# Kernel optimization log

Measured on AMD Instinct MI355X. Metric: run time of the kernel, lower is better.

Reference implementation:

```python
import jax, jax.numpy as jnp
import numpy as np

B, S, E, H = 4, 4096, 1024, 16
D = E // H  # head_dim = 64


def _xavier(key, out_f, in_f):
    lim = float(np.sqrt(6.0 / (in_f + out_f)))
    return jax.random.uniform(key, (out_f, in_f), jnp.float32, -lim, lim)


def setup_inputs() -> dict:
    key = jax.random.key(0)
    ks = jax.random.split(key, 9)
    x = jax.random.normal(ks[0], (B, S, E), jnp.float32)
    Wq = _xavier(ks[1], E, E)
    Wk = _xavier(ks[2], E, E)
    Wv = _xavier(ks[3], E, E)
    Wo = _xavier(ks[4], E, E)
    bq = jnp.zeros((E,), jnp.float32)
    bk = jnp.zeros((E,), jnp.float32)
    bv = jnp.zeros((E,), jnp.float32)
    bo = jnp.zeros((E,), jnp.float32)
    return {"x": x, "Wq": Wq, "bq": bq, "Wk": Wk, "bk": bk,
            "Wv": Wv, "bv": bv, "Wo": Wo, "bo": bo}


def _feature_map(t):
    # elu(t) + 1 (positive feature map)
    return jax.nn.elu(t) + 1.0


def reference(x, Wq, bq, Wk, bk, Wv, bv, Wo, bo):
    b, s, _ = x.shape
    # projections (torch Linear: y = x @ W.T + b), reshape to [b, s, h, d]
    Q = (x @ Wq.T + bq).reshape(b, s, H, D)
    K = (x @ Wk.T + bk).reshape(b, s, H, D)
    V = (x @ Wv.T + bv).reshape(b, s, H, D)
    Q = _feature_map(Q)
    K = _feature_map(K)
    # KV summary: [b, h, d, e]
    KV = jnp.einsum('bshd,bshe->bhde', K, V)
    K_sum = K.sum(axis=1)  # [b, h, d]
    Z = 1.0 / (jnp.einsum('bshd,bhd->bsh', Q, K_sum) + 1e-6)  # [b, s, h]
    out = jnp.einsum('bshd,bhde,bsh->bshe', Q, KV, Z)  # [b, s, h, e]
    out = out.reshape(b, s, E)
    out = out @ Wo.T + bo
    return out
```

## Files before the change

kernel.cpp:

```cpp
#include <hip/hip_runtime.h>
#include <math.h>

#define BB 4
#define SS 4096
#define EE 1024
#define HH 16
#define DD 64
#define MM (BB*SS)

typedef _Float16 f16x8 __attribute__((ext_vector_type(8)));
typedef _Float16 f16x4 __attribute__((ext_vector_type(4)));
typedef float    f32x4 __attribute__((ext_vector_type(4)));

typedef __attribute__((address_space(3))) void lds_void;
typedef __attribute__((address_space(1))) void gm_void;

__device__ __forceinline__ void gload16(const void* g, void* l) {
  __builtin_amdgcn_global_load_lds((gm_void*)g, (lds_void*)l, 16, 0, 0);
}

__global__ __launch_bounds__(256) void conv_x_kernel(const float* __restrict__ x,
                                                     _Float16* __restrict__ xh, int n4) {
  int i = blockIdx.x * blockDim.x + threadIdx.x;
  int stride = gridDim.x * blockDim.x;
  for (; i < n4; i += stride) {
    f32x4 v = *(const f32x4*)&x[(size_t)i * 4];
    f16x4 h;
    h[0] = (_Float16)v[0]; h[1] = (_Float16)v[1];
    h[2] = (_Float16)v[2]; h[3] = (_Float16)v[3];
    *(f16x4*)&xh[(size_t)i * 4] = h;
  }
}

__global__ __launch_bounds__(256) void conv_w_kernel(const float* __restrict__ Wq,
                                                     const float* __restrict__ Wk,
                                                     const float* __restrict__ Wv,
                                                     const float* __restrict__ Wo,
                                                     _Float16* __restrict__ wqkv,
                                                     _Float16* __restrict__ woh) {
  const int per = (EE * EE) / 4;
  int i = blockIdx.x * blockDim.x + threadIdx.x;
  int stride = gridDim.x * blockDim.x;
  for (; i < 4 * per; i += stride) {
    int seg = i / per, off = i - seg * per;
    const float* src = (seg == 0) ? Wq : (seg == 1) ? Wk : (seg == 2) ? Wv : Wo;
    _Float16* dst = (seg < 3) ? (wqkv + (size_t)seg * EE * EE) : woh;
    f32x4 v = *(const f32x4*)&src[(size_t)off * 4];
    f16x4 h;
    h[0] = (_Float16)v[0]; h[1] = (_Float16)v[1];
    h[2] = (_Float16)v[2]; h[3] = (_Float16)v[3];
    *(f16x4*)&dst[(size_t)off * 4] = h;
  }
}


#define SB0() __builtin_amdgcn_sched_barrier(0)
#define VMW6 asm volatile("s_waitcnt vmcnt(6)" ::: "memory")
#define VMW0 asm volatile("s_waitcnt vmcnt(0)" ::: "memory")
#define NOP_ do {} while (0)

#define STAGE_M(Gb, Lb, t, hf) do {                                          \
    const char* g_ = (Gb) + ((size_t)(hf) << 18) + (size_t)(t) * 128;        \
    char* d_ = (Lb) + (((t) & 1) << 15) + ((hf) << 14) + dsub;               \
    gload16(g_, d_);                                                         \
    gload16(g_ + ((size_t)64 << 11), d_ + 8192);                             \
  } while (0)

#define STAGE_A(t, hf) STAGE_M(Ag, Asb, t, hf)
#define STAGE_B(t, hf) STAGE_M(Bg, Bsb, t, hf)

#define RD_A(mf, s) (*(const f16x8*)(Asb + buf_ +                            \
    (((((mf) < 4) ? 0 : 8) + wr4 + ((mf) & 3)) << 11) + ((s) << 10) + lof))
#define RD_B(nf, s) (*(const f16x8*)(Bsb + buf_ + ((wc4 + (nf)) << 11) + ((s) << 10) + lof))

#define PHASE(t, P, STG, VMC) do {                                           \
    const int buf_ = ((t) & 1) << 15;                                        \
    if ((P) == 0) {                                                          \
      _Pragma("unroll") for (int nf = 0; nf < 4; nf++) {                     \
        b[nf][0] = RD_B(nf, 0); b[nf][1] = RD_B(nf, 1);                      \
      }                                                                      \
    }                                                                        \
    aP[0][0] = RD_A((P) * 2, 0);     aP[0][1] = RD_A((P) * 2, 1);            \
    aP[1][0] = RD_A((P) * 2 + 1, 0); aP[1][1] = RD_A((P) * 2 + 1, 1);        \
    STG;                                                                     \
    SB0(); __builtin_amdgcn_s_barrier(); SB0();                              \
    asm volatile("s_waitcnt lgkmcnt(0)" ::: "memory"); SB0();                \
    __builtin_amdgcn_s_setprio(1);                                           \
    _Pragma("unroll") for (int nf = 0; nf < 4; nf++) {                       \
      acc[(P)*2][nf]   = __builtin_amdgcn_mfma_f32_16x16x32_f16(aP[0][0], b[nf][0], acc[(P)*2][nf], 0, 0, 0);   \
      acc[(P)*2][nf]   = __builtin_amdgcn_mfma_f32_16x16x32_f16(aP[0][1], b[nf][1], acc[(P)*2][nf], 0, 0, 0);   \
      acc[(P)*2+1][nf] = __builtin_amdgcn_mfma_f32_16x16x32_f16(aP[1][0], b[nf][0], acc[(P)*2+1][nf], 0, 0, 0); \
      acc[(P)*2+1][nf] = __builtin_amdgcn_mfma_f32_16x16x32_f16(aP[1][1], b[nf][1], acc[(P)*2+1][nf], 0, 0, 0); \
    }                                                                        \
    __builtin_amdgcn_s_setprio(0);                                           \
    VMC;                                                                     \
    SB0(); __builtin_amdgcn_s_barrier(); SB0();                              \
  } while (0)

#define TILE(t, S1, S2, S3, S4, VMC) do {                                    \
    PHASE(t, 0, S1, NOP_);                                                   \
    PHASE(t, 1, S2, NOP_);                                                   \
    PHASE(t, 2, S3, NOP_);                                                   \
    PHASE(t, 3, S4, VMC);                                                    \
  } while (0)

template <int EPI>
__global__ __launch_bounds__(512, 2) void gemm256(const _Float16* __restrict__ A,
                                                  const _Float16* __restrict__ Bw,
                                                  const float* __restrict__ bias0,
                                                  const float* __restrict__ bias1,
                                                  const float* __restrict__ bias2,
                                                  _Float16* __restrict__ O0,
                                                  _Float16* __restrict__ O1,
                                                  _Float16* __restrict__ O2,
                                                  float* __restrict__ OF) {
  __shared__ __align__(16) char lds[131072];
  char* Asb = lds;
  char* Bsb = lds + 65536;

  const int tid  = threadIdx.x;
  const int lane = tid & 63;
  const int wv   = tid >> 6;
  const int wr4  = (wv >> 2) << 2;
  const int wc4  = (wv & 3) << 2;
  const int wrow = (wv >> 2) << 6;
  const int wcol = (wv & 3) << 6;

  constexpr int NX = (EPI == 0) ? 12 : 4;
  const int q = (int)gridDim.x >> 3;
  const int bid = (int)blockIdx.x;
  const int sid = (bid & 7) * q + (bid >> 3);
  const int mbase = (sid / NX) << 8;
  const int nbase = (sid % NX) << 8;

  const int lof   = (((lane & 15) << 6) | ((lane >> 4) << 4)) ^ ((lane & 8) << 2);
  const int srow  = lane >> 2;
  const int sbyte = ((lane & 3) << 4) ^ (lane & 32);

  const int rg   = wv >> 1;
  const int kgs  = wv & 1;
  const int dsub = ((rg << 1) + kgs) << 10;

  const char* Ag = (const char*)A +
      ((size_t)(mbase + (rg << 4) + srow) << 11) + (kgs << 6) + sbyte;
  const char* Bg = (const char*)Bw +
      ((size_t)(nbase + (rg << 4) + srow) << 11) + (kgs << 6) + sbyte;

  f32x4 acc[8][4] = {};
  f16x8 b[4][2];
  f16x8 aP[2][2];

  STAGE_A(0, 0); STAGE_A(0, 1);
  STAGE_B(0, 0); STAGE_B(0, 1);
  STAGE_B(1, 0); STAGE_B(1, 1);
  STAGE_A(1, 0);
  VMW6;
  SB0(); __builtin_amdgcn_s_barrier(); SB0();

#pragma unroll 1
  for (int i = 0; i < 7; ++i) {
    const int t = i << 1;
    TILE(t,     STAGE_A(t + 1, 1), STAGE_B(t + 2, 0), STAGE_B(t + 2, 1), STAGE_A(t + 2, 0), VMW6);
    TILE(t + 1, STAGE_A(t + 2, 1), STAGE_B(t + 3, 0), STAGE_B(t + 3, 1), STAGE_A(t + 3, 0), VMW6);
  }
  TILE(14, STAGE_A(15, 1), NOP_, NOP_, NOP_, VMW0);
  TILE(15, NOP_, NOP_, NOP_, NOP_, NOP_);

  const int rl = (lane >> 4) << 2;
  const int cl = lane & 15;
  if (EPI == 0) {
    const int which = nbase >> 10;
    const float* bias = (which == 0) ? bias0 : (which == 1) ? bias1 : bias2;
    _Float16* O = (which == 0) ? O0 : (which == 1) ? O1 : O2;
    const int cb = (nbase & 1023) + wcol;
#pragma unroll
    for (int mf = 0; mf < 8; mf++) {
      const int gm = mbase + ((mf < 4) ? 0 : 128) + wrow + ((mf & 3) << 4) + rl;
#pragma unroll
      for (int nf = 0; nf < 4; nf++) {
        const int gc = cb + (nf << 4) + cl;
        const float bz = bias[gc];
#pragma unroll
        for (int j = 0; j < 4; j++) {
          float v = acc[mf][nf][j] + bz;
          if (which < 2) v = (v > 0.f) ? (v + 1.f) : expf(v);
          O[(size_t)(gm + j) * EE + gc] = (_Float16)v;
        }
      }
    }
  } else {
    const int cb = nbase + wcol;
#pragma unroll
    for (int mf = 0; mf < 8; mf++) {
      const int gm = mbase + ((mf < 4) ? 0 : 128) + wrow + ((mf & 3) << 4) + rl;
#pragma unroll
      for (int nf = 0; nf < 4; nf++) {
        const int gc = cb + (nf << 4) + cl;
        const float bz = bias0[gc];
#pragma unroll
        for (int j = 0; j < 4; j++)
          OF[(size_t)(gm + j) * EE + gc] = acc[mf][nf][j] + bz;
      }
    }
  }
}

#undef TILE
#undef PHASE
#undef RD_A
#undef RD_B
#undef STAGE_A
#undef STAGE_B
#undef STAGE_M

__global__ __launch_bounds__(256) void kv_partial_kernel(const _Float16* __restrict__ Kh,
                                                         const _Float16* __restrict__ Vh,
                                                         float* __restrict__ kvpart,
                                                         float* __restrict__ ksump) {
  __shared__ __align__(16) _Float16 Ks[64 * 64];
  __shared__ __align__(16) _Float16 Vs[64 * 64];
  const int tid = threadIdx.x;
  const int wv = tid >> 6;
  const int bh = blockIdx.x;
  const int chunk = blockIdx.y;
  const int b = bh >> 4, h = bh & 15;
  const int td = tid >> 4, te = tid & 15;
  const int d0 = td * 4, e0 = te * 4;

  float kv[4][4] = {};
  float ks4[4] = {0.f, 0.f, 0.f, 0.f};

  for (int sub = 0; sub < 4; sub++) {
    const int s0 = chunk * 256 + sub * 64;
    __syncthreads();
    {
      const int g0 = tid, g1 = tid + 256;
      gload16((const char*)Kh + ((size_t)(b * SS + s0 + (g0 >> 3)) * EE + h * DD) * 2 + (g0 & 7) * 16,
              (char*)Ks + wv * 1024);
      gload16((const char*)Kh + ((size_t)(b * SS + s0 + (g1 >> 3)) * EE + h * DD) * 2 + (g1 & 7) * 16,
              (char*)Ks + 4096 + wv * 1024);
      gload16((const char*)Vh + ((size_t)(b * SS + s0 + (g0 >> 3)) * EE + h * DD) * 2 + (g0 & 7) * 16,
              (char*)Vs + wv * 1024);
      gload16((const char*)Vh + ((size_t)(b * SS + s0 + (g1 >> 3)) * EE + h * DD) * 2 + (g1 & 7) * 16,
              (char*)Vs + 4096 + wv * 1024);
    }
    __syncthreads();
#pragma unroll 8
    for (int s = 0; s < 64; s++) {
      f16x4 kk = *(const f16x4*)&Ks[s * 64 + d0];
      f16x4 vv = *(const f16x4*)&Vs[s * 64 + e0];
      float kf[4], vf[4];
#pragma unroll
      for (int i = 0; i < 4; i++) { kf[i] = (float)kk[i]; vf[i] = (float)vv[i]; }
#pragma unroll
      for (int i = 0; i < 4; i++)
#pragma unroll
        for (int j = 0; j < 4; j++) kv[i][j] += kf[i] * vf[j];
      if (te == 0) {
#pragma unroll
        for (int i = 0; i < 4; i++) ks4[i] += kf[i];
      }
    }
  }
  const size_t base = ((size_t)chunk * 64 + bh) * 4096;
#pragma unroll
  for (int i = 0; i < 4; i++)
#pragma unroll
    for (int j = 0; j < 4; j++) kvpart[base + (size_t)(d0 + i) * 64 + e0 + j] = kv[i][j];
  if (te == 0) {
#pragma unroll
    for (int i = 0; i < 4; i++) ksump[((size_t)chunk * 64 + bh) * 64 + d0 + i] = ks4[i];
  }
}

__global__ __launch_bounds__(256) void kv_reduce_kernel(const float* __restrict__ kvpart,
                                                        const float* __restrict__ ksump,
                                                        _Float16* __restrict__ kvt,
                                                        float* __restrict__ ksum) {
  const int idx = blockIdx.x * 256 + threadIdx.x;
  if (blockIdx.x < 1024) {
    const int bh = idx >> 12;
    const int rem = idx & 4095;
    float s = 0.f;
#pragma unroll
    for (int c = 0; c < 16; c++) s += kvpart[((size_t)c * 64 + bh) * 4096 + rem];
    const int d = rem >> 6, e = rem & 63;
    kvt[(size_t)bh * 4096 + e * 64 + d] = (_Float16)s;
  } else {
    const int i2 = idx - 1024 * 256;
    const int bh = i2 >> 6, d = i2 & 63;
    float s = 0.f;
#pragma unroll
    for (int c = 0; c < 16; c++) s += ksump[((size_t)c * 64 + bh) * 64 + d];
    ksum[i2] = s;
  }
}

__global__ __launch_bounds__(256) void attn_kernel(const _Float16* __restrict__ Qh,
                                                   const _Float16* __restrict__ kvt,
                                                   const float* __restrict__ ksum,
                                                   _Float16* __restrict__ attn) {
  __shared__ __align__(16) _Float16 Qs[64 * 64];
  __shared__ __align__(16) _Float16 KVs[64 * 64];
  __shared__ float ks_lds[64];
  __shared__ float dpart[4][64];
  __shared__ float zr[64];
  const int tid = threadIdx.x;
  const int lane = tid & 63;
  const int wv = tid >> 6;
  const int stile = blockIdx.x;
  const int bh = blockIdx.y;
  const int b = bh >> 4, h = bh & 15;
  const int m0 = b * SS + stile * 64;

  {
    const int g0 = tid, g1 = tid + 256;
    gload16((const char*)Qh + ((size_t)(m0 + (g0 >> 3)) * EE + h * DD) * 2 + (g0 & 7) * 16,
            (char*)Qs + wv * 1024);
    gload16((const char*)Qh + ((size_t)(m0 + (g1 >> 3)) * EE + h * DD) * 2 + (g1 & 7) * 16,
            (char*)Qs + 4096 + wv * 1024);
    gload16((const char*)kvt + (size_t)bh * 8192 + (size_t)g0 * 16, (char*)KVs + wv * 1024);
    gload16((const char*)kvt + (size_t)bh * 8192 + (size_t)g1 * 16, (char*)KVs + 4096 + wv * 1024);
  }
  if (tid < 64) ks_lds[tid] = ksum[bh * 64 + tid];
  __syncthreads();

  {
    const int r = tid & 63, qd = tid >> 6;
    float p = 0.f;
#pragma unroll
    for (int i = 0; i < 16; i++) p += (float)Qs[r * 64 + qd * 16 + i] * ks_lds[qd * 16 + i];
    dpart[qd][r] = p;
  }
  __syncthreads();
  if (tid < 64) {
    float den = dpart[0][tid] + dpart[1][tid] + dpart[2][tid] + dpart[3][tid];
    zr[tid] = 1.f / (den + 1e-6f);
  }
  __syncthreads();

  f32x4 acc[4] = {};
  const int fr = lane & 15;
  const int kg = (lane >> 4) * 8;
#pragma unroll
  for (int kh = 0; kh < 2; kh++) {
    f16x8 a = *(const f16x8*)&Qs[(wv * 16 + fr) * 64 + kh * 32 + kg];
#pragma unroll
    for (int n = 0; n < 4; n++) {
      f16x8 b8 = *(const f16x8*)&KVs[(n * 16 + fr) * 64 + kh * 32 + kg];
      acc[n] = __builtin_amdgcn_mfma_f32_16x16x32_f16(a, b8, acc[n], 0, 0, 0);
    }
  }

  const int rl = (lane >> 4) * 4, cl = lane & 15;
#pragma unroll
  for (int n = 0; n < 4; n++)
#pragma unroll
    for (int j = 0; j < 4; j++) {
      const int r = wv * 16 + rl + j;
      float v = acc[n][j] * zr[r];
      attn[(size_t)(m0 + r) * EE + h * DD + n * 16 + cl] = (_Float16)v;
    }
}

extern "C" void kernel_launch(void* const* d_in, const int* in_sizes, int n_in,
                              void* d_out, int out_size, void* d_ws, size_t ws_size,
                              hipStream_t stream) {
  const float* x  = (const float*)d_in[0];
  const float* Wq = (const float*)d_in[1];
  const float* bq = (const float*)d_in[2];
  const float* Wk = (const float*)d_in[3];
  const float* bk = (const float*)d_in[4];
  const float* Wv = (const float*)d_in[5];
  const float* bv = (const float*)d_in[6];
  const float* Wo = (const float*)d_in[7];
  const float* bo = (const float*)d_in[8];
  float* out = (float*)d_out;

  char* ws = (char*)d_ws;
  size_t off = 0;
  auto alloc = [&](size_t bytes) -> char* {
    char* p = ws + off;
    off += (bytes + 255) & ~(size_t)255;
    return p;
  };
  _Float16* xh    = (_Float16*)alloc((size_t)MM * EE * 2);
  _Float16* wqkv  = (_Float16*)alloc((size_t)3 * EE * EE * 2);
  _Float16* woh   = (_Float16*)alloc((size_t)EE * EE * 2);
  _Float16* Qh    = (_Float16*)alloc((size_t)MM * EE * 2);
  _Float16* Kh    = (_Float16*)alloc((size_t)MM * EE * 2);
  _Float16* Vh    = (_Float16*)alloc((size_t)MM * EE * 2);
  float*    kvpart= (float*)alloc((size_t)16 * 64 * 4096 * 4);
  float*    ksump = (float*)alloc((size_t)16 * 64 * 64 * 4);
  _Float16* kvt   = (_Float16*)alloc((size_t)64 * 4096 * 2);
  float*    ksum  = (float*)alloc((size_t)64 * 64 * 4);
  _Float16* attn  = xh;

  (void)in_sizes; (void)n_in; (void)out_size; (void)ws_size;

  conv_x_kernel<<<2048, 256, 0, stream>>>(x, xh, (MM * EE) / 4);
  conv_w_kernel<<<1024, 256, 0, stream>>>(Wq, Wk, Wv, Wo, wqkv, woh);
  gemm256<0><<<768, 512, 0, stream>>>(xh, wqkv, bq, bk, bv, Qh, Kh, Vh, nullptr);
  kv_partial_kernel<<<dim3(64, 16), 256, 0, stream>>>(Kh, Vh, kvpart, ksump);
  kv_reduce_kernel<<<1040, 256, 0, stream>>>(kvpart, ksump, kvt, ksum);
  attn_kernel<<<dim3(64, 64), 256, 0, stream>>>(Qh, kvt, ksum, attn);
  gemm256<1><<<256, 512, 0, stream>>>(attn, woh, bo, nullptr, nullptr,
                                      nullptr, nullptr, nullptr, out);
}
```

Measured before the change: 253.3 us.

## Restructure GEMM mainloop to 4-stage K=32 ring buffer with one barrier per tile

Replaces the GEMM main loop, which used two K=64 buffers split into four phases with two barriers each, with a four-deep ring of K=32 tiles. Each tile loads all A and B fragments, issues the next-but-one stage's global-to-LDS loads, runs 32 MFMAs, then waits and does a single barrier. The LDS swizzle and the wave-to-tile mapping change to match. This is meant to cut barrier and phase overhead and deepen prefetch, but it drops the s_setprio interleaving and uses a shorter K step per barrier.

```diff
diff --git a/kernel.cpp b/kernel.cpp
--- a/kernel.cpp
+++ b/kernel.cpp
@@ -54,54 +54,36 @@
 }
 
 
-#define SB0() __builtin_amdgcn_sched_barrier(0)
-#define VMW6 asm volatile("s_waitcnt vmcnt(6)" ::: "memory")
+#define SCB() __builtin_amdgcn_sched_barrier(0)
+#define VMW4 asm volatile("s_waitcnt vmcnt(4)" ::: "memory")
 #define VMW0 asm volatile("s_waitcnt vmcnt(0)" ::: "memory")
+#define BARR do { SCB(); __builtin_amdgcn_s_barrier(); SCB(); } while (0)
 #define NOP_ do {} while (0)
 
-#define STAGE_M(Gb, Lb, t, hf) do {                                          \
-    const char* g_ = (Gb) + ((size_t)(hf) << 18) + (size_t)(t) * 128;        \
-    char* d_ = (Lb) + (((t) & 1) << 15) + ((hf) << 14) + dsub;               \
-    gload16(g_, d_);                                                         \
-    gload16(g_ + ((size_t)64 << 11), d_ + 8192);                             \
-  } while (0)
-
-#define STAGE_A(t, hf) STAGE_M(Ag, Asb, t, hf)
-#define STAGE_B(t, hf) STAGE_M(Bg, Bsb, t, hf)
-
-#define RD_A(mf, s) (*(const f16x8*)(Asb + buf_ +                            \
-    (((((mf) < 4) ? 0 : 8) + wr4 + ((mf) & 3)) << 11) + ((s) << 10) + lof))
-#define RD_B(nf, s) (*(const f16x8*)(Bsb + buf_ + ((wc4 + (nf)) << 11) + ((s) << 10) + lof))
-
-#define PHASE(t, P, STG, VMC) do {                                           \
-    const int buf_ = ((t) & 1) << 15;                                        \
-    if ((P) == 0) {                                                          \
-      _Pragma("unroll") for (int nf = 0; nf < 4; nf++) {                     \
-        b[nf][0] = RD_B(nf, 0); b[nf][1] = RD_B(nf, 1);                      \
-      }                                                                      \
+#define STAGE_A(t, h) gload16(Ag + (size_t)(h) * 262144 + (size_t)(t) * 64,  \
+                              LdsA + (((t) & 3) << 14) + ((h) << 13) + wvb)
+#define STAGE_B(t, h) gload16(Bg + (size_t)(h) * 262144 + (size_t)(t) * 64,  \
+                              LdsB + (((t) & 3) << 14) + ((h) << 13) + wvb)
+#define STG4(t2) do { STAGE_A(t2, 0); STAGE_A(t2, 1);                        \
+                      STAGE_B(t2, 0); STAGE_B(t2, 1); } while (0)
+
+#define RD_A(bb, mf) (*(const f16x8*)(LdsA + ((bb) << 14) + wrb + ((mf) << 10) + lof))
+#define RD_B(bb, nf) (*(const f16x8*)(LdsB + ((bb) << 14) + wcb + ((nf) << 10) + lof))
+
+#define TILE_(t, STG, VW, BAR) do {                                          \
+    const int bb = (t) & 3;                                                  \
+    f16x8 Bf0 = RD_B(bb, 0), Bf1 = RD_B(bb, 1);                              \
+    f16x8 Bf2 = RD_B(bb, 2), Bf3 = RD_B(bb, 3);                              \
+    f16x8 Af[8];                                                             \
+    _Pragma("unroll") for (int mf = 0; mf < 8; mf++) Af[mf] = RD_A(bb, mf);  \
+    STG;                                                                     \
+    _Pragma("unroll") for (int mf = 0; mf < 8; mf++) {                       \
+      acc[mf][0] = __builtin_amdgcn_mfma_f32_16x16x32_f16(Af[mf], Bf0, acc[mf][0], 0, 0, 0); \
+      acc[mf][1] = __builtin_amdgcn_mfma_f32_16x16x32_f16(Af[mf], Bf1, acc[mf][1], 0, 0, 0); \
+      acc[mf][2] = __builtin_amdgcn_mfma_f32_16x16x32_f16(Af[mf], Bf2, acc[mf][2], 0, 0, 0); \
+      acc[mf][3] = __builtin_amdgcn_mfma_f32_16x16x32_f16(Af[mf], Bf3, acc[mf][3], 0, 0, 0); \
     }                                                                        \
-    aP[0][0] = RD_A((P) * 2, 0);     aP[0][1] = RD_A((P) * 2, 1);            \
-    aP[1][0] = RD_A((P) * 2 + 1, 0); aP[1][1] = RD_A((P) * 2 + 1, 1);        \
-    STG;                                                                     \
-    SB0(); __builtin_amdgcn_s_barrier(); SB0();                              \
-    asm volatile("s_waitcnt lgkmcnt(0)" ::: "memory"); SB0();                \
-    __builtin_amdgcn_s_setprio(1);                                           \
-    _Pragma("unroll") for (int nf = 0; nf < 4; nf++) {                       \
-      acc[(P)*2][nf]   = __builtin_amdgcn_mfma_f32_16x16x32_f16(aP[0][0], b[nf][0], acc[(P)*2][nf], 0, 0, 0);   \
-      acc[(P)*2][nf]   = __builtin_amdgcn_mfma_f32_16x16x32_f16(aP[0][1], b[nf][1], acc[(P)*2][nf], 0, 0, 0);   \
-      acc[(P)*2+1][nf] = __builtin_amdgcn_mfma_f32_16x16x32_f16(aP[1][0], b[nf][0], acc[(P)*2+1][nf], 0, 0, 0); \
-      acc[(P)*2+1][nf] = __builtin_amdgcn_mfma_f32_16x16x32_f16(aP[1][1], b[nf][1], acc[(P)*2+1][nf], 0, 0, 0); \
-    }                                                                        \
-    __builtin_amdgcn_s_setprio(0);                                           \
-    VMC;                                                                     \
-    SB0(); __builtin_amdgcn_s_barrier(); SB0();                              \
-  } while (0)
-
-#define TILE(t, S1, S2, S3, S4, VMC) do {                                    \
-    PHASE(t, 0, S1, NOP_);                                                   \
-    PHASE(t, 1, S2, NOP_);                                                   \
-    PHASE(t, 2, S3, NOP_);                                                   \
-    PHASE(t, 3, S4, VMC);                                                    \
+    VW; BAR;                                                                 \
   } while (0)
 
 template <int EPI>
@@ -115,16 +97,17 @@
                                                   _Float16* __restrict__ O2,
                                                   float* __restrict__ OF) {
   __shared__ __align__(16) char lds[131072];
-  char* Asb = lds;
-  char* Bsb = lds + 65536;
+  char* LdsA = lds;
+  char* LdsB = lds + 65536;
 
   const int tid  = threadIdx.x;
   const int lane = tid & 63;
   const int wv   = tid >> 6;
-  const int wr4  = (wv >> 2) << 2;
-  const int wc4  = (wv & 3) << 2;
-  const int wrow = (wv >> 2) << 6;
-  const int wcol = (wv & 3) << 6;
+  const int wr   = wv >> 2;
+  const int wc   = wv & 3;
+  const int wvb  = wv << 10;
+  const int wrb  = wr << 13;
+  const int wcb  = wc << 12;
 
   constexpr int NX = (EPI == 0) ? 12 : 4;
   const int q = (int)gridDim.x >> 3;
@@ -133,49 +116,41 @@
   const int mbase = (sid / NX) << 8;
   const int nbase = (sid % NX) << 8;
 
-  const int lof   = (((lane & 15) << 6) | ((lane >> 4) << 4)) ^ ((lane & 8) << 2);
-  const int srow  = lane >> 2;
-  const int sbyte = ((lane & 3) << 4) ^ (lane & 32);
-
-  const int rg   = wv >> 1;
-  const int kgs  = wv & 1;
-  const int dsub = ((rg << 1) + kgs) << 10;
-
-  const char* Ag = (const char*)A +
-      ((size_t)(mbase + (rg << 4) + srow) << 11) + (kgs << 6) + sbyte;
-  const char* Bg = (const char*)Bw +
-      ((size_t)(nbase + (rg << 4) + srow) << 11) + (kgs << 6) + sbyte;
+  const int lof = ((lane & 15) << 6) + (((lane >> 4) ^ ((lane >> 1) & 3)) << 4);
+  const int plane = ((lane >> 2) << 11) + (((lane & 3) ^ ((lane >> 3) & 3)) << 4);
+
+  const char* Ag = (const char*)A + ((size_t)(mbase + wv * 16) << 11) + plane;
+  const char* Bg = (const char*)Bw + ((size_t)(nbase + wv * 16) << 11) + plane;
 
   f32x4 acc[8][4] = {};
-  f16x8 b[4][2];
-  f16x8 aP[2][2];
-
-  STAGE_A(0, 0); STAGE_A(0, 1);
-  STAGE_B(0, 0); STAGE_B(0, 1);
-  STAGE_B(1, 0); STAGE_B(1, 1);
-  STAGE_A(1, 0);
-  VMW6;
-  SB0(); __builtin_amdgcn_s_barrier(); SB0();
+
+  STG4(0); STG4(1);
+  VMW4; BARR;
 
 #pragma unroll 1
   for (int i = 0; i < 7; ++i) {
-    const int t = i << 1;
-    TILE(t,     STAGE_A(t + 1, 1), STAGE_B(t + 2, 0), STAGE_B(t + 2, 1), STAGE_A(t + 2, 0), VMW6);
-    TILE(t + 1, STAGE_A(t + 2, 1), STAGE_B(t + 3, 0), STAGE_B(t + 3, 1), STAGE_A(t + 3, 0), VMW6);
-  }
-  TILE(14, STAGE_A(15, 1), NOP_, NOP_, NOP_, VMW0);
-  TILE(15, NOP_, NOP_, NOP_, NOP_, NOP_);
+    const int t = i << 2;
+    TILE_(t + 0, STG4(t + 2), VMW4, BARR);
+    TILE_(t + 1, STG4(t + 3), VMW4, BARR);
+    TILE_(t + 2, STG4(t + 4), VMW4, BARR);
+    TILE_(t + 3, STG4(t + 5), VMW4, BARR);
+  }
+  TILE_(28, STG4(30), VMW4, BARR);
+  TILE_(29, STG4(31), VMW4, BARR);
+  TILE_(30, NOP_, VMW0, BARR);
+  TILE_(31, NOP_, NOP_, NOP_);
 
   const int rl = (lane >> 4) << 2;
   const int cl = lane & 15;
+  const int rb = mbase + (wr << 7);
   if (EPI == 0) {
     const int which = nbase >> 10;
     const float* bias = (which == 0) ? bias0 : (which == 1) ? bias1 : bias2;
     _Float16* O = (which == 0) ? O0 : (which == 1) ? O1 : O2;
-    const int cb = (nbase & 1023) + wcol;
+    const int cb = (nbase & 1023) + (wc << 6);
 #pragma unroll
     for (int mf = 0; mf < 8; mf++) {
-      const int gm = mbase + ((mf < 4) ? 0 : 128) + wrow + ((mf & 3) << 4) + rl;
+      const int gm = rb + (mf << 4) + rl;
 #pragma unroll
       for (int nf = 0; nf < 4; nf++) {
         const int gc = cb + (nf << 4) + cl;
@@ -189,10 +164,10 @@
       }
     }
   } else {
-    const int cb = nbase + wcol;
+    const int cb = nbase + (wc << 6);
 #pragma unroll
     for (int mf = 0; mf < 8; mf++) {
-      const int gm = mbase + ((mf < 4) ? 0 : 128) + wrow + ((mf & 3) << 4) + rl;
+      const int gm = rb + (mf << 4) + rl;
 #pragma unroll
       for (int nf = 0; nf < 4; nf++) {
         const int gc = cb + (nf << 4) + cl;
@@ -205,13 +180,12 @@
   }
 }
 
-#undef TILE
-#undef PHASE
+#undef TILE_
 #undef RD_A
 #undef RD_B
+#undef STG4
 #undef STAGE_A
 #undef STAGE_B
-#undef STAGE_M
 
 __global__ __launch_bounds__(256) void kv_partial_kernel(const _Float16* __restrict__ Kh,
                                                          const _Float16* __restrict__ Vh,
```

Result: slower. 261.5 us (+3.2%).
